# Kernel tuning notes

Measured on AMD Instinct MI355X. Metric: run time of the kernel, lower is better.

The kernel has to match this reference:

```python
import jax, jax.numpy as jnp
import numpy as np

N_NODES = 50000
N_EDGES = 800000
IN_FT = 128
HID_FT = 64
EMB_FT = 128
NUM_LAYERS = 4
NEG_SLOP = 0.2


def setup_inputs() -> dict:
    key = jax.random.key(0)
    ks = jax.random.split(key, 16)
    x = jax.random.normal(ks[0], (N_NODES, IN_FT), dtype=jnp.float32)
    edge_index = jax.random.randint(ks[1], (2, N_EDGES), 0, N_NODES, dtype=jnp.int64)
    edge_weight = jax.random.uniform(ks[2], (N_EDGES,), dtype=jnp.float32)
    def lin(k, fin, fout):
        s = 1.0 / np.sqrt(fin)
        kw, kb = jax.random.split(k)
        W = jax.random.uniform(kw, (fin, fout), minval=-s, maxval=s, dtype=jnp.float32)
        b = jax.random.uniform(kb, (fout,), minval=-s, maxval=s, dtype=jnp.float32)
        return W, b
    W1, b1 = lin(ks[3], IN_FT, HID_FT)
    W2, b2 = lin(ks[4], HID_FT, HID_FT)
    W3, b3 = lin(ks[5], HID_FT, HID_FT)
    W4, b4 = lin(ks[6], HID_FT, HID_FT)
    Wh, bh = lin(ks[7], NUM_LAYERS * HID_FT, EMB_FT)
    return {"x": x, "edge_index": edge_index, "edge_weight": edge_weight,
            "W1": W1, "b1": b1, "W2": W2, "b2": b2, "W3": W3, "b3": b3,
            "W4": W4, "b4": b4, "Wh": Wh, "bh": bh}


def _gcn_no_norm(x, src, dst, ew, W, b):
    # GCNConv(add_self_loops=False, normalize=False): plain weighted scatter-add
    h = x @ W                                   # [N, F]
    msg = h[src] * ew[:, None]                  # gather over edges [E, F]
    return jax.ops.segment_sum(msg, dst, num_segments=N_NODES) + b


def _gcn_norm(x, src, dst, ew, W, b):
    # Default GCNConv: add self loops (weight 1) + symmetric normalization.
    deg = jax.ops.segment_sum(ew, dst, num_segments=N_NODES) + 1.0  # +1 self loop
    dinv = jnp.where(deg > 0, jax.lax.rsqrt(deg), 0.0)
    norm = dinv[src] * ew * dinv[dst]           # [E]
    h = x @ W
    agg = jax.ops.segment_sum(h[src] * norm[:, None], dst, num_segments=N_NODES)
    agg = agg + (dinv * dinv)[:, None] * h      # self-loop term
    return agg + b


def _forward(x, edge_index, edge_weight, W1, b1, W2, b2, W3, b3, W4, b4, Wh, bh):
    src, dst = edge_index[0], edge_index[1]
    lrelu = lambda v: jax.nn.leaky_relu(v, NEG_SLOP)
    outs = []
    h = lrelu(_gcn_no_norm(x, src, dst, edge_weight, W1, b1))
    outs.append(h)  # dropout is identity in deterministic reference
    for W, b in ((W2, b2), (W3, b3), (W4, b4)):
        h = lrelu(_gcn_norm(h, src, dst, edge_weight, W, b))
        outs.append(h)
    cat = jnp.concatenate(outs, axis=-1)        # [N, num_layers*HID_FT]
    return cat @ Wh + bh


def reference(x, edge_index, edge_weight, W1, b1, W2, b2, W3, b3, W4, b4, Wh, bh):
    return _forward(x, edge_index, edge_weight, W1, b1, W2, b2, W3, b3, W4, b4, Wh, bh)
```

## Files before the change

### kernel.cpp

```cpp
#include <hip/hip_runtime.h>
#include <hip/hip_bf16.h>

#define NEG_SLOP 0.2f
typedef unsigned long long ull;
typedef __attribute__((ext_vector_type(8))) short bf16x8;
typedef __attribute__((ext_vector_type(4))) float f32x4;

__device__ __forceinline__ float lrelu(float v) { return v > 0.0f ? v : NEG_SLOP * v; }

__device__ __forceinline__ float bf2f(unsigned short u) {
    union { unsigned int i; float f; } c; c.i = ((unsigned int)u) << 16; return c.f;
}
__device__ __forceinline__ unsigned short f2bf(float f) {
    union { float f; unsigned int i; } c; c.f = f;
    unsigned int r = c.i + 0x7FFF + ((c.i >> 16) & 1);
    return (unsigned short)(r >> 16);
}

struct us8 { ushort4 a, b; };

__global__ void prep_kernel(const float* __restrict__ Wh, unsigned short* __restrict__ wht,
                            const float* __restrict__ W1, unsigned short* __restrict__ w1t,
                            const float* __restrict__ W2, unsigned short* __restrict__ w2t,
                            const float* __restrict__ W3, unsigned short* __restrict__ w3t,
                            const float* __restrict__ W4, unsigned short* __restrict__ w4t,
                            float4* __restrict__ pz, int nz) {
    int idx = blockIdx.x * 256 + threadIdx.x;
    if (idx < nz) pz[idx] = make_float4(0.f, 0.f, 0.f, 0.f);
    if (idx < 256 * 128) {
        int k = idx >> 7, c = idx & 127;
        wht[(size_t)c * 256 + k] = f2bf(Wh[idx]);
    }
    if (idx < 64 * 128) {
        int c = idx >> 7, k = idx & 127;
        w1t[idx] = f2bf(W1[k * 64 + c]);
    }
    if (idx < 64 * 64) {
        int c = idx >> 6, k = idx & 63;
        w2t[idx] = f2bf(W2[k * 64 + c]);
        w3t[idx] = f2bf(W3[k * 64 + c]);
        w4t[idx] = f2bf(W4[k * 64 + c]);
    }
}

__global__ void histo_kernel(const int* __restrict__ dst, const float* __restrict__ ew,
                             ull* __restrict__ packed4, int* __restrict__ rank,
                             int n_edges, int n) {
    int e = blockIdx.x * 256 + threadIdx.x;
    if (e >= n_edges) return;
    int d = dst[e];
    int c = e & 3;
    ull delta = (1ULL << 40) | (ull)(ew[e] * 4294967296.0f);
    ull old = atomicAdd(&packed4[(size_t)c * n + d], delta);
    rank[e] = (int)(old >> 40);
}

__global__ void scan1_kernel(const ull* __restrict__ packed4, int* __restrict__ pre,
                             int4* __restrict__ bases, int* __restrict__ bsum,
                             float* __restrict__ dinv, int n) {
    __shared__ int s[256];
    int t = threadIdx.x;
    int base = blockIdx.x * 1024 + t * 4;
    const ull m = (1ULL << 40) - 1;
    int tot[4];
#pragma unroll
    for (int j = 0; j < 4; ++j) {
        int node = base + j;
        if (node < n) {
            ull p0 = packed4[node];
            ull p1 = packed4[(size_t)n + node];
            ull p2 = packed4[2 * (size_t)n + node];
            ull p3 = packed4[3 * (size_t)n + node];
            int c0 = (int)(p0 >> 40), c1 = (int)(p1 >> 40);
            int c2 = (int)(p2 >> 40), c3 = (int)(p3 >> 40);
            bases[node] = make_int4(0, c0, c0 + c1, c0 + c1 + c2);
            tot[j] = c0 + c1 + c2 + c3;
            float deg = (float)((p0 & m) + (p1 & m) + (p2 & m) + (p3 & m)) *
                        (1.0f / 4294967296.0f);
            dinv[node] = rsqrtf(deg + 1.0f);
        } else tot[j] = 0;
    }
    int tsum = tot[0] + tot[1] + tot[2] + tot[3];
    s[t] = tsum;
    __syncthreads();
    for (int off = 1; off < 256; off <<= 1) {
        int v = (t >= off) ? s[t - off] : 0;
        __syncthreads();
        s[t] += v;
        __syncthreads();
    }
    int ex = s[t] - tsum;
    if (t == 255) bsum[blockIdx.x] = s[255];
    int o[4];
    o[0] = ex; o[1] = ex + tot[0]; o[2] = o[1] + tot[1]; o[3] = o[2] + tot[2];
    if (base + 3 < n) *(int4*)&pre[base] = make_int4(o[0], o[1], o[2], o[3]);
    else {
        for (int j = 0; j < 4; ++j) if (base + j < n) pre[base + j] = o[j];
    }
}

__global__ void scan2_kernel(int* __restrict__ bsum, int nb) {
    __shared__ int s[64];
    int t = threadIdx.x;
    int v = (t < nb) ? bsum[t] : 0;
    s[t] = v;
    __syncthreads();
    for (int off = 1; off < 64; off <<= 1) {
        int u = (t >= off) ? s[t - off] : 0;
        __syncthreads();
        s[t] += u;
        __syncthreads();
    }
    if (t < nb) bsum[t] = s[t] - v;
}

__global__ void scan3_kernel(int* __restrict__ rp, const int* __restrict__ bsum,
                             int n, int n_edges) {
    int t = blockIdx.x * 256 + threadIdx.x;
    int base = t * 4;
    if (base >= n) {
        if (base == ((n + 3) & ~3)) rp[n] = n_edges;
        return;
    }
    int boff = bsum[base >> 10];
    if (base + 3 < n) {
        int4 v = *(const int4*)&rp[base];
        v.x += boff; v.y += boff; v.z += boff; v.w += boff;
        *(int4*)&rp[base] = v;
    } else {
        for (int j = 0; j < 4 && base + j < n; ++j) rp[base + j] += boff;
        rp[n] = n_edges;
    }
}

__global__ void fill_kernel(const int* __restrict__ src, const int* __restrict__ dst,
                            const float* __restrict__ ew, const int* __restrict__ rank,
                            const int* __restrict__ rp, const int4* __restrict__ bases,
                            int2* __restrict__ e_sw, int n_edges) {
    int e = blockIdx.x * 256 + threadIdx.x;
    if (e >= n_edges) return;
    int d = dst[e];
    int c = e & 3;
    int4 bs = bases[d];
    int b = (c == 0) ? bs.x : (c == 1) ? bs.y : (c == 2) ? bs.z : bs.w;
    int pos = rp[d] + b + rank[e];
    e_sw[pos] = make_int2(src[e], __float_as_int(ew[e]));
}

__global__ void gather_plain(const int* __restrict__ rp, const int2* __restrict__ e_sw,
                             const unsigned short* __restrict__ hb,
                             const float* __restrict__ b, unsigned short* __restrict__ cat, int n) {
    int node = (blockIdx.x * 256 + threadIdx.x) >> 6;
    if (node >= n) return;
    int lane = threadIdx.x & 63;
    int eg = lane >> 3;
    int f0 = (lane & 7) * 8;
    int lo = rp[node], hi = rp[node + 1];
    float a[8] = {};
    for (int k = lo + eg; k < hi; k += 16) {
        int k1 = k + 8;
        int2 p0 = e_sw[k];
        int2 p1 = e_sw[k1 < hi ? k1 : k];
        float w0 = __int_as_float(p0.y);
        float w1 = k1 < hi ? __int_as_float(p1.y) : 0.f;
        us8 u0 = *(const us8*)&hb[(size_t)p0.x * 64 + f0];
        us8 u1 = *(const us8*)&hb[(size_t)p1.x * 64 + f0];
        a[0] += w0 * bf2f(u0.a.x) + w1 * bf2f(u1.a.x);
        a[1] += w0 * bf2f(u0.a.y) + w1 * bf2f(u1.a.y);
        a[2] += w0 * bf2f(u0.a.z) + w1 * bf2f(u1.a.z);
        a[3] += w0 * bf2f(u0.a.w) + w1 * bf2f(u1.a.w);
        a[4] += w0 * bf2f(u0.b.x) + w1 * bf2f(u1.b.x);
        a[5] += w0 * bf2f(u0.b.y) + w1 * bf2f(u1.b.y);
        a[6] += w0 * bf2f(u0.b.z) + w1 * bf2f(u1.b.z);
        a[7] += w0 * bf2f(u0.b.w) + w1 * bf2f(u1.b.w);
    }
#pragma unroll
    for (int j = 0; j < 8; ++j) {
        a[j] += __shfl_xor(a[j], 8, 64);
        a[j] += __shfl_xor(a[j], 16, 64);
        a[j] += __shfl_xor(a[j], 32, 64);
    }
    if (eg == 0) {
        unsigned short o[8];
#pragma unroll
        for (int j = 0; j < 8; ++j) o[j] = f2bf(lrelu(a[j] + b[f0 + j]));
        *(int4*)&cat[(size_t)node * 256 + f0] = *(int4*)o;
    }
}

__global__ void gather_norm(const int* __restrict__ rp, const int2* __restrict__ e_sw,
                            const unsigned short* __restrict__ hb,
                            const float* __restrict__ dinv, const float* __restrict__ b,
                            unsigned short* __restrict__ cat, int col_off, int n) {
    int node = (blockIdx.x * 256 + threadIdx.x) >> 6;
    if (node >= n) return;
    int lane = threadIdx.x & 63;
    int eg = lane >> 3;
    int f0 = (lane & 7) * 8;
    int lo = rp[node], hi = rp[node + 1];
    float a[8] = {};
    for (int k = lo + eg; k < hi; k += 16) {
        int k1 = k + 8;
        int2 p0 = e_sw[k];
        int2 p1 = e_sw[k1 < hi ? k1 : k];
        float w0 = __int_as_float(p0.y);
        float w1 = k1 < hi ? __int_as_float(p1.y) : 0.f;
        us8 u0 = *(const us8*)&hb[(size_t)p0.x * 64 + f0];
        us8 u1 = *(const us8*)&hb[(size_t)p1.x * 64 + f0];
        a[0] += w0 * bf2f(u0.a.x) + w1 * bf2f(u1.a.x);
        a[1] += w0 * bf2f(u0.a.y) + w1 * bf2f(u1.a.y);
        a[2] += w0 * bf2f(u0.a.z) + w1 * bf2f(u1.a.z);
        a[3] += w0 * bf2f(u0.a.w) + w1 * bf2f(u1.a.w);
        a[4] += w0 * bf2f(u0.b.x) + w1 * bf2f(u1.b.x);
        a[5] += w0 * bf2f(u0.b.y) + w1 * bf2f(u1.b.y);
        a[6] += w0 * bf2f(u0.b.z) + w1 * bf2f(u1.b.z);
        a[7] += w0 * bf2f(u0.b.w) + w1 * bf2f(u1.b.w);
    }
#pragma unroll
    for (int j = 0; j < 8; ++j) {
        a[j] += __shfl_xor(a[j], 8, 64);
        a[j] += __shfl_xor(a[j], 16, 64);
        a[j] += __shfl_xor(a[j], 32, 64);
    }
    if (eg == 0) {
        float di = dinv[node];
        us8 h = *(const us8*)&hb[(size_t)node * 64 + f0];
        float hs[8] = {bf2f(h.a.x), bf2f(h.a.y), bf2f(h.a.z), bf2f(h.a.w),
                       bf2f(h.b.x), bf2f(h.b.y), bf2f(h.b.z), bf2f(h.b.w)};
        unsigned short o[8];
#pragma unroll
        for (int j = 0; j < 8; ++j) o[j] = f2bf(lrelu(di * (a[j] + hs[j]) + b[f0 + j]));
        *(int4*)&cat[(size_t)node * 256 + col_off + f0] = *(int4*)o;
    }
}

__global__ __launch_bounds__(256) void gemm_hid_mfma(
    const unsigned short* __restrict__ in, int in_stride,
    const unsigned short* __restrict__ wT, const float* __restrict__ dinv,
    unsigned short* __restrict__ outb, int n_rows) {
    __shared__ __align__(16) char As[64 * 128];
    __shared__ __align__(16) char Bs[64 * 128];
    const int tid = threadIdx.x;
    const int wid = tid >> 6, lane = tid & 63;
    const int row0 = blockIdx.x * 64;
    const int lrow = lane & 15, kg = lane >> 4;
    {
        int row = tid >> 2, seg = tid & 3;
        int rr = row0 + row; if (rr >= n_rows) rr = n_rows - 1;
        const int4* g = (const int4*)&in[(size_t)rr * in_stride + seg * 16];
        int4 u0 = g[0], u1 = g[1];
        const int4* gb = (const int4*)&wT[(size_t)row * 64 + seg * 16];
        int4 v0 = gb[0], v1 = gb[1];
        int sw = (row & 7) << 4;
        int base = row * 128 + seg * 32;
        *(int4*)(As + (base ^ sw)) = u0;
        *(int4*)(As + ((base + 16) ^ sw)) = u1;
        *(int4*)(Bs + (base ^ sw)) = v0;
        *(int4*)(Bs + ((base + 16) ^ sw)) = v1;
    }
    __syncthreads();
    int arow = wid * 16 + lrow;
    int asw = (arow & 7) << 4;
    f32x4 acc[4] = {};
#pragma unroll
    for (int ks = 0; ks < 2; ++ks) {
        bf16x8 af = *(bf16x8*)(As + ((arow * 128 + ks * 64 + kg * 16) ^ asw));
#pragma unroll
        for (int cf = 0; cf < 4; ++cf) {
            int c = cf * 16 + lrow;
            bf16x8 bf = *(bf16x8*)(Bs + ((c * 128 + ks * 64 + kg * 16) ^ ((c & 7) << 4)));
            acc[cf] = __builtin_amdgcn_mfma_f32_16x16x32_bf16(af, bf, acc[cf], 0, 0, 0);
        }
    }
    int r4 = (lane >> 4) * 4;
#pragma unroll
    for (int reg = 0; reg < 4; ++reg) {
        int r = row0 + wid * 16 + r4 + reg;
        if (r >= n_rows) continue;
        float di = dinv[r];
#pragma unroll
        for (int cf = 0; cf < 4; ++cf)
            outb[(size_t)r * 64 + cf * 16 + lrow] = f2bf(acc[cf][reg] * di);
    }
}

__global__ __launch_bounds__(256) void gemm_hid_mfma_x(
    const float* __restrict__ x, const unsigned short* __restrict__ w1T,
    unsigned short* __restrict__ outb, int n_rows) {
    __shared__ __align__(16) char As[64 * 256];
    __shared__ __align__(16) char Bs[64 * 256];
    const int tid = threadIdx.x;
    const int wid = tid >> 6, lane = tid & 63;
    const int row0 = blockIdx.x * 64;
    const int lrow = lane & 15, kg = lane >> 4;
    {
        int row = tid >> 2, seg = tid & 3;
        int rr = row0 + row; if (rr >= n_rows) rr = n_rows - 1;
        const float4* g = (const float4*)&x[(size_t)rr * 128 + seg * 32];
        const int4* gb = (const int4*)&w1T[(size_t)row * 128 + seg * 32];
        int sw = (row & 7) << 4;
        int base = row * 256 + seg * 64;
#pragma unroll
        for (int i = 0; i < 4; ++i) {
            float4 f0 = g[2 * i], f1 = g[2 * i + 1];
            unsigned short u[8] = {f2bf(f0.x), f2bf(f0.y), f2bf(f0.z), f2bf(f0.w),
                                   f2bf(f1.x), f2bf(f1.y), f2bf(f1.z), f2bf(f1.w)};
            *(int4*)(As + ((base + i * 16) ^ sw)) = *(int4*)u;
            *(int4*)(Bs + ((base + i * 16) ^ sw)) = gb[i];
        }
    }
    __syncthreads();
    int arow = wid * 16 + lrow;
    int asw = (arow & 7) << 4;
    f32x4 acc[4] = {};
#pragma unroll
    for (int ks = 0; ks < 4; ++ks) {
        bf16x8 af = *(bf16x8*)(As + ((arow * 256 + ks * 64 + kg * 16) ^ asw));
#pragma unroll
        for (int cf = 0; cf < 4; ++cf) {
            int c = cf * 16 + lrow;
            bf16x8 bf = *(bf16x8*)(Bs + ((c * 256 + ks * 64 + kg * 16) ^ ((c & 7) << 4)));
            acc[cf] = __builtin_amdgcn_mfma_f32_16x16x32_bf16(af, bf, acc[cf], 0, 0, 0);
        }
    }
    int r4 = (lane >> 4) * 4;
#pragma unroll
    for (int reg = 0; reg < 4; ++reg) {
        int r = row0 + wid * 16 + r4 + reg;
        if (r >= n_rows) continue;
#pragma unroll
        for (int cf = 0; cf < 4; ++cf)
            outb[(size_t)r * 64 + cf * 16 + lrow] = f2bf(acc[cf][reg]);
    }
}

__global__ __launch_bounds__(256) void gemm_out_mfma(
    const unsigned short* __restrict__ cat, const unsigned short* __restrict__ whT,
    const float* __restrict__ bh, float* __restrict__ out, int n_rows) {
    __shared__ __align__(16) char As[64 * 128];
    __shared__ __align__(16) char Bs[128 * 128];
    const int tid = threadIdx.x;
    const int wid = tid >> 6, lane = tid & 63;
    const int row0 = blockIdx.x * 64;
    const int lrow = lane & 15, kg = lane >> 4;
    f32x4 acc[8] = {};
    for (int kc = 0; kc < 4; ++kc) {
        __syncthreads();
        {
            int row = tid >> 2, seg = tid & 3;
            int rr = row0 + row; if (rr >= n_rows) rr = n_rows - 1;
            const int4* g = (const int4*)&cat[(size_t)rr * 256 + kc * 64 + seg * 16];
            int4 u0 = g[0], u1 = g[1];
            int sw = (row & 7) << 4;
            int base = row * 128 + seg * 32;
            *(int4*)(As + (base ^ sw)) = u0;
            *(int4*)(As + ((base + 16) ^ sw)) = u1;
        }
        {
            int c = tid >> 1, seg = tid & 1;
            const int4* g = (const int4*)&whT[(size_t)c * 256 + kc * 64 + seg * 32];
            int sw = (c & 7) << 4;
            int base = c * 128 + seg * 64;
#pragma unroll
            for (int i = 0; i < 4; ++i)
                *(int4*)(Bs + ((base + i * 16) ^ sw)) = g[i];
        }
        __syncthreads();
        int arow = wid * 16 + lrow;
        int asw = (arow & 7) << 4;
#pragma unroll
        for (int ks = 0; ks < 2; ++ks) {
            bf16x8 af = *(bf16x8*)(As + ((arow * 128 + ks * 64 + kg * 16) ^ asw));
#pragma unroll
            for (int cf = 0; cf < 8; ++cf) {
                int c = cf * 16 + lrow;
                bf16x8 bf = *(bf16x8*)(Bs + ((c * 128 + ks * 64 + kg * 16) ^ ((c & 7) << 4)));
                acc[cf] = __builtin_amdgcn_mfma_f32_16x16x32_bf16(af, bf, acc[cf], 0, 0, 0);
            }
        }
    }
    int lrow4 = (lane >> 4) * 4;
#pragma unroll
    for (int cf = 0; cf < 8; ++cf) {
        int col = cf * 16 + lrow;
        float bias = bh[col];
#pragma unroll
        for (int reg = 0; reg < 4; ++reg) {
            int r = row0 + wid * 16 + lrow4 + reg;
            if (r < n_rows) out[(size_t)r * 128 + col] = acc[cf][reg] + bias;
        }
    }
}

extern "C" void kernel_launch(void* const* d_in, const int* in_sizes, int n_in,
                              void* d_out, int out_size, void* d_ws, size_t ws_size,
                              hipStream_t stream) {
    const float* x  = (const float*)d_in[0];
    const int*   ei = (const int*)d_in[1];
    const float* ew = (const float*)d_in[2];
    const float* W1 = (const float*)d_in[3];
    const float* b1 = (const float*)d_in[4];
    const float* W2 = (const float*)d_in[5];
    const float* b2 = (const float*)d_in[6];
    const float* W3 = (const float*)d_in[7];
    const float* b3 = (const float*)d_in[8];
    const float* W4 = (const float*)d_in[9];
    const float* b4 = (const float*)d_in[10];
    const float* Wh = (const float*)d_in[11];
    const float* bh = (const float*)d_in[12];

    const int E = in_sizes[2];
    const int N = in_sizes[0] / 128;
    const int* src = ei;
    const int* dst = ei + E;

    char* p = (char*)d_ws;
    unsigned short* cat     = (unsigned short*)p; p += (size_t)N * 256 * 2;
    unsigned short* hb      = (unsigned short*)p; p += (size_t)N * 64 * 2;
    unsigned short* wht     = (unsigned short*)p; p += (size_t)128 * 256 * 2;
    unsigned short* w1t     = (unsigned short*)p; p += (size_t)64 * 128 * 2;
    unsigned short* w2t     = (unsigned short*)p; p += (size_t)64 * 64 * 2;
    unsigned short* w3t     = (unsigned short*)p; p += (size_t)64 * 64 * 2;
    unsigned short* w4t     = (unsigned short*)p; p += (size_t)64 * 64 * 2;
    ull*            packed4 = (ull*)p;            p += (size_t)N * 4 * 8;
    float*          dinv    = (float*)p;          p += (size_t)N * 4;
    int*            row_ptr = (int*)p;            p += (size_t)(N + 4) * 4;
    int*            bsum    = (int*)p;            p += (size_t)64 * 4;
    int4*           bases   = (int4*)p;           p += (size_t)N * 16;
    int*            rank    = (int*)p;            p += (size_t)E * 4;
    int2*           e_sw    = (int2*)p;           p += (size_t)E * 8;
    float* out = (float*)d_out;

    int eb   = (E + 255) / 256;
    int nb64 = (N * 64 + 255) / 256;
    int gb64 = (N + 63) / 64;
    int sb   = (N + 1023) / 1024;
    int s3b  = ((N + 3) / 4 + 256) / 256;
    int nz   = N * 2;
    int pb   = (nz > 256 * 128 ? nz : 256 * 128) / 256 + 1;

    prep_kernel<<<pb, 256, 0, stream>>>(Wh, wht, W1, w1t, W2, w2t, W3, w3t, W4, w4t,
                                        (float4*)packed4, nz);
    histo_kernel<<<eb, 256, 0, stream>>>(dst, ew, packed4, rank, E, N);
    scan1_kernel<<<sb, 256, 0, stream>>>(packed4, row_ptr, bases, bsum, dinv, N);
    scan2_kernel<<<1, 64, 0, stream>>>(bsum, sb);
    scan3_kernel<<<s3b, 256, 0, stream>>>(row_ptr, bsum, N, E);
    fill_kernel<<<eb, 256, 0, stream>>>(src, dst, ew, rank, row_ptr, bases, e_sw, E);

    gemm_hid_mfma_x<<<gb64, 256, 0, stream>>>(x, w1t, hb, N);
    gather_plain<<<nb64, 256, 0, stream>>>(row_ptr, e_sw, hb, b1, cat, N);

    const unsigned short* Wt[3] = {w2t, w3t, w4t};
    const float* bl[3] = {b2, b3, b4};
    for (int l = 1; l < 4; ++l) {
        gemm_hid_mfma<<<gb64, 256, 0, stream>>>(cat + (size_t)(l - 1) * 64, 256,
                                                Wt[l - 1], dinv, hb, N);
        gather_norm<<<nb64, 256, 0, stream>>>(row_ptr, e_sw, hb, dinv,
                                              bl[l - 1], cat, l * 64, N);
    }

    gemm_out_mfma<<<gb64, 256, 0, stream>>>(cat, wht, bh, out, N);
}
```

Measured before the change: 213.3 us.

## Fuse block-sum scan into scan3, prefold row offsets into bases, nontemporal edge loads

The single-block scan2 kernel is removed. Each scan3 block now redundantly scans the up-to-64 block sums in shared memory. scan3 also adds the final row pointer into the per-node bases, so fill_kernel no longer has to read row_ptr per edge. The gather kernels load edge records with nontemporal hints and hoist the self-loop h and dinv loads ahead of the edge loop to overlap their latency. The trade-off is extra base read-modify-write traffic in scan3 and a possible cache-policy effect from the nontemporal loads.

After: 224.1 us. 5.1% more time.

```diff
diff --git a/kernel.cpp b/kernel.cpp
--- a/kernel.cpp
+++ b/kernel.cpp
@@ -18,6 +18,11 @@
 }
 
 struct us8 { ushort4 a, b; };
+
+__device__ __forceinline__ int2 ld_nt_i2(const int2* p) {
+    long long v = __builtin_nontemporal_load((const long long*)p);
+    int2 r; r.x = (int)(v & 0xffffffffLL); r.y = (int)(v >> 32); return r;
+}
 
 __global__ void prep_kernel(const float* __restrict__ Wh, unsigned short* __restrict__ wht,
                             const float* __restrict__ W1, unsigned short* __restrict__ w1t,
@@ -99,43 +104,56 @@
     }
 }
 
-__global__ void scan2_kernel(int* __restrict__ bsum, int nb) {
-    __shared__ int s[64];
+__global__ void scan3_kernel(int* __restrict__ rp, int4* __restrict__ bases,
+                             const int* __restrict__ bsum, int nbsum,
+                             int n, int n_edges) {
+    __shared__ int sb[64];
+    __shared__ int boffs[64];
     int t = threadIdx.x;
-    int v = (t < nb) ? bsum[t] : 0;
-    s[t] = v;
+    int myv = 0;
+    if (t < 64) { myv = (t < nbsum) ? bsum[t] : 0; sb[t] = myv; }
     __syncthreads();
     for (int off = 1; off < 64; off <<= 1) {
-        int u = (t >= off) ? s[t - off] : 0;
-        __syncthreads();
-        s[t] += u;
-        __syncthreads();
-    }
-    if (t < nb) bsum[t] = s[t] - v;
-}
-
-__global__ void scan3_kernel(int* __restrict__ rp, const int* __restrict__ bsum,
-                             int n, int n_edges) {
-    int t = blockIdx.x * 256 + threadIdx.x;
-    int base = t * 4;
+        int u = (t >= off && t < 64) ? sb[t - off] : 0;
+        __syncthreads();
+        if (t < 64) sb[t] += u;
+        __syncthreads();
+    }
+    if (t < 64) boffs[t] = sb[t] - myv;
+    __syncthreads();
+    int idx = blockIdx.x * 256 + t;
+    int base = idx * 4;
     if (base >= n) {
         if (base == ((n + 3) & ~3)) rp[n] = n_edges;
         return;
     }
-    int boff = bsum[base >> 10];
+    int boff = boffs[(base >> 10) & 63];
     if (base + 3 < n) {
-        int4 v = *(const int4*)&rp[base];
+        int4 v = *(int4*)&rp[base];
         v.x += boff; v.y += boff; v.z += boff; v.w += boff;
         *(int4*)&rp[base] = v;
+        int va[4] = {v.x, v.y, v.z, v.w};
+#pragma unroll
+        for (int j = 0; j < 4; ++j) {
+            int4 bs = bases[base + j];
+            bs.x += va[j]; bs.y += va[j]; bs.z += va[j]; bs.w += va[j];
+            bases[base + j] = bs;
+        }
     } else {
-        for (int j = 0; j < 4 && base + j < n; ++j) rp[base + j] += boff;
+        for (int j = 0; j < 4 && base + j < n; ++j) {
+            int v = rp[base + j] + boff;
+            rp[base + j] = v;
+            int4 bs = bases[base + j];
+            bs.x += v; bs.y += v; bs.z += v; bs.w += v;
+            bases[base + j] = bs;
+        }
         rp[n] = n_edges;
     }
 }
 
 __global__ void fill_kernel(const int* __restrict__ src, const int* __restrict__ dst,
                             const float* __restrict__ ew, const int* __restrict__ rank,
-                            const int* __restrict__ rp, const int4* __restrict__ bases,
+                            const int4* __restrict__ bases,
                             int2* __restrict__ e_sw, int n_edges) {
     int e = blockIdx.x * 256 + threadIdx.x;
     if (e >= n_edges) return;
@@ -143,8 +161,7 @@
     int c = e & 3;
     int4 bs = bases[d];
     int b = (c == 0) ? bs.x : (c == 1) ? bs.y : (c == 2) ? bs.z : bs.w;
-    int pos = rp[d] + b + rank[e];
-    e_sw[pos] = make_int2(src[e], __float_as_int(ew[e]));
+    e_sw[b + rank[e]] = make_int2(src[e], __float_as_int(ew[e]));
 }
 
 __global__ void gather_plain(const int* __restrict__ rp, const int2* __restrict__ e_sw,
@@ -159,8 +176,8 @@
     float a[8] = {};
     for (int k = lo + eg; k < hi; k += 16) {
         int k1 = k + 8;
-        int2 p0 = e_sw[k];
-        int2 p1 = e_sw[k1 < hi ? k1 : k];
+        int2 p0 = ld_nt_i2(&e_sw[k]);
+        int2 p1 = ld_nt_i2(&e_sw[k1 < hi ? k1 : k]);
         float w0 = __int_as_float(p0.y);
         float w1 = k1 < hi ? __int_as_float(p1.y) : 0.f;
         us8 u0 = *(const us8*)&hb[(size_t)p0.x * 64 + f0];
@@ -197,12 +214,14 @@
     int lane = threadIdx.x & 63;
     int eg = lane >> 3;
     int f0 = (lane & 7) * 8;
+    float di = dinv[node];
+    us8 h = *(const us8*)&hb[(size_t)node * 64 + f0];
     int lo = rp[node], hi = rp[node + 1];
     float a[8] = {};
     for (int k = lo + eg; k < hi; k += 16) {
         int k1 = k + 8;
-        int2 p0 = e_sw[k];
-        int2 p1 = e_sw[k1 < hi ? k1 : k];
+        int2 p0 = ld_nt_i2(&e_sw[k]);
+        int2 p1 = ld_nt_i2(&e_sw[k1 < hi ? k1 : k]);
         float w0 = __int_as_float(p0.y);
         float w1 = k1 < hi ? __int_as_float(p1.y) : 0.f;
         us8 u0 = *(const us8*)&hb[(size_t)p0.x * 64 + f0];
@@ -223,8 +242,6 @@
         a[j] += __shfl_xor(a[j], 32, 64);
     }
     if (eg == 0) {
-        float di = dinv[node];
-        us8 h = *(const us8*)&hb[(size_t)node * 64 + f0];
         float hs[8] = {bf2f(h.a.x), bf2f(h.a.y), bf2f(h.a.z), bf2f(h.a.w),
                        bf2f(h.b.x), bf2f(h.b.y), bf2f(h.b.z), bf2f(h.b.w)};
         unsigned short o[8];
@@ -443,9 +460,8 @@
                                         (float4*)packed4, nz);
     histo_kernel<<<eb, 256, 0, stream>>>(dst, ew, packed4, rank, E, N);
     scan1_kernel<<<sb, 256, 0, stream>>>(packed4, row_ptr, bases, bsum, dinv, N);
-    scan2_kernel<<<1, 64, 0, stream>>>(bsum, sb);
-    scan3_kernel<<<s3b, 256, 0, stream>>>(row_ptr, bsum, N, E);
-    fill_kernel<<<eb, 256, 0, stream>>>(src, dst, ew, rank, row_ptr, bases, e_sw, E);
+    scan3_kernel<<<s3b, 256, 0, stream>>>(row_ptr, bases, bsum, sb, N, E);
+    fill_kernel<<<eb, 256, 0, stream>>>(src, dst, ew, rank, bases, e_sw, E);
 
     gemm_hid_mfma_x<<<gb64, 256, 0, stream>>>(x, w1t, hb, N);
     gather_plain<<<nb64, 256, 0, stream>>>(row_ptr, e_sw, hb, b1, cat, N);
```
